# Kernel tuning notes

Measured on AMD Instinct MI355X. Metric: run time of the kernel, lower is better.

Reference implementation:

```python
import jax, jax.numpy as jnp
import numpy as np

B, T, C = 16, 64, 512


def setup_inputs() -> dict:
    key = jax.random.key(0)
    ks = jax.random.split(key, 12)
    s = 1.0 / np.sqrt(C)
    st = 1.0 / np.sqrt(2.0)
    return {
        "x": jax.random.normal(ks[0], (B, T, C), dtype=jnp.float32),
        "ts": jax.random.uniform(ks[1], (B, T), dtype=jnp.float32),
        "attn_mask": jnp.ones((B, T), dtype=jnp.float32),
        # project: Linear(C, C)
        "W_proj": jax.random.uniform(ks[2], (C, C), jnp.float32, -s, s),
        "b_proj": jax.random.uniform(ks[3], (C,), jnp.float32, -s, s),
        # embed_xs: Linear(C, C)
        "W_x": jax.random.uniform(ks[4], (C, C), jnp.float32, -s, s),
        "b_x": jax.random.uniform(ks[5], (C,), jnp.float32, -s, s),
        # embed_ts: Linear(2, C)
        "W_t": jax.random.uniform(ks[6], (2, C), jnp.float32, -st, st),
        "b_t": jax.random.uniform(ks[7], (C,), jnp.float32, -st, st),
        # get_importances Linear(C, C)
        "W_imp": jax.random.uniform(ks[8], (C, C), jnp.float32, -s, s),
        "b_imp": jax.random.uniform(ks[9], (C,), jnp.float32, -s, s),
    }


def reference(x, ts, attn_mask, W_proj, b_proj, W_x, b_x, W_t, b_t, W_imp, b_imp):
    # x: [B,T,C], ts: [B,T], attn_mask: [B,T]
    values = (x @ W_proj + b_proj)[:, None, :, :]          # [B,1,T,C]
    rel = ts[:, :, None] - ts[:, None, :]                  # [B,T,T]
    rel2 = jnp.log1p(jnp.maximum(jnp.stack([rel, -rel], axis=-1), 0.0))  # [B,T,T,2]
    h = rel2 @ W_t + b_t                                   # [B,T,T,C] (include_t)
    h = h + (x @ W_x + b_x)[:, None, :, :]                 # include_x, broadcast over dim 1
    importances = jax.nn.sigmoid(jax.nn.relu(h) @ W_imp + b_imp)  # [B,T,T,C]
    importances = importances * attn_mask[:, None, :, None]
    interactions = jax.nn.logsumexp(values * importances, axis=2)  # [B,T,C]
    return (x + interactions, importances.mean(axis=3))
```

## Files before the change

kernel.cpp:

```cpp
#include <hip/hip_runtime.h>
#include <hip/hip_bf16.h>

#define Bn 16
#define Tn 64
#define Cn 512
#define LDA 520

#define LOG2E 1.4426950408889634f
#define LN2   0.6931471805599453f

typedef short s8v __attribute__((ext_vector_type(8)));
typedef float f4v __attribute__((ext_vector_type(4)));

__device__ __forceinline__ unsigned short f2bf(float f){
  union { float f; unsigned int u; } c; c.f = f;
  return (unsigned short)((c.u + 0x7FFFu + ((c.u >> 16) & 1u)) >> 16);
}
__device__ __forceinline__ unsigned int pk2bf(float a, float b){
  __hip_bfloat162 t = __float22bfloat162_rn(make_float2(a, b));
  union { __hip_bfloat162 h; unsigned int u; } c; c.h = t; return c.u;
}
__device__ __forceinline__ float bits2f(unsigned int u){
  union { unsigned int u; float f; } c; c.u = u; return c.f;
}

__global__ void swz(const float* __restrict__ Wp, const float* __restrict__ Wx,
                    const float* __restrict__ Wi, const float* __restrict__ ts,
                    unsigned short* __restrict__ dstall, float* __restrict__ R){
  if(blockIdx.x < 384){
    int gid = blockIdx.x * 256 + threadIdx.x;
    int mat = gid >> 15;
    int rem = gid & 32767;
    int lane = rem & 63;
    int st   = rem >> 6;
    int t    = st & 31;
    int s    = st >> 5;
    int n  = t * 16 + (lane & 15);
    int k0 = s * 32 + ((lane >> 4) << 3);
    const float* W = (mat == 0) ? Wp : ((mat == 1) ? Wx : Wi);
    unsigned int p[4];
#pragma unroll
    for(int q = 0; q < 4; ++q)
      p[q] = pk2bf(W[(k0 + 2*q) * Cn + n], W[(k0 + 2*q + 1) * Cn + n]);
    uint4 o; o.x = p[0]; o.y = p[1]; o.z = p[2]; o.w = p[3];
    *reinterpret_cast<uint4*>(dstall + (size_t)mat * 262144 + (size_t)rem * 8) = o;
  } else {
    int gid2 = (blockIdx.x - 384) * 256 + threadIdx.x;
    float r[8];
#pragma unroll
    for(int q = 0; q < 4; ++q){
      int p = gid2 * 4 + q;
      int b = p >> 12, i = (p >> 6) & 63, j = p & 63;
      float d = ts[b * Tn + i] - ts[b * Tn + j];
      r[2*q]   = __logf(1.f + fmaxf(d, 0.f));
      r[2*q+1] = __logf(1.f + fmaxf(-d, 0.f));
    }
    float4* Rf4 = reinterpret_cast<float4*>(R);
    Rf4[gid2 * 2    ] = make_float4(r[0], r[1], r[2], r[3]);
    Rf4[gid2 * 2 + 1] = make_float4(r[4], r[5], r[6], r[7]);
  }
}

__global__ __launch_bounds__(256, 4)
void prep(const float* __restrict__ x, const float* __restrict__ bp,
          const float* __restrict__ bx, const float* __restrict__ bt,
          const unsigned short* __restrict__ WswP,
          const unsigned short* __restrict__ WswX,
          float* __restrict__ xe, unsigned short* __restrict__ vfrag){
  __shared__ unsigned short lA[Tn * LDA];
  const int b = blockIdx.x >> 2, mat = (blockIdx.x >> 1) & 1, half = blockIdx.x & 1;
  const int tid = threadIdx.x;
  const int c0 = (tid & 127) * 4, jb = tid >> 7;
#pragma unroll
  for(int it = 0; it < 32; ++it){
    int j = jb + it * 2;
    f4v xv = *reinterpret_cast<const f4v*>(x + ((b * Tn + j) * Cn + c0));
    uint2 uu; uu.x = pk2bf(xv[0], xv[1]); uu.y = pk2bf(xv[2], xv[3]);
    *reinterpret_cast<uint2*>(&lA[j * LDA + c0]) = uu;
  }
  __syncthreads();
  const unsigned short* Wsw = mat ? WswX : WswP;
  const int lane = tid & 63, w2 = tid >> 6, quad = lane >> 4, ln = lane & 15;
  const int wg = half * 4 + w2;
  f4v acc[4][4];
#pragma unroll
  for(int mt = 0; mt < 4; ++mt)
#pragma unroll
    for(int nt = 0; nt < 4; ++nt){
      acc[mt][nt][0] = 0.f; acc[mt][nt][1] = 0.f; acc[mt][nt][2] = 0.f; acc[mt][nt][3] = 0.f;
    }
#pragma unroll 1
  for(int s = 0; s < 16; ++s){
    s8v af[4], bfv[4];
#pragma unroll
    for(int mt = 0; mt < 4; ++mt)
      af[mt] = *reinterpret_cast<const s8v*>(&lA[(mt * 16 + ln) * LDA + s * 32 + quad * 8]);
#pragma unroll
    for(int nt = 0; nt < 4; ++nt)
      bfv[nt] = *reinterpret_cast<const s8v*>(Wsw + (((s * 32) + (wg * 4 + nt)) * 64 + lane) * 8);
#pragma unroll
    for(int mt = 0; mt < 4; ++mt)
#pragma unroll
      for(int nt = 0; nt < 4; ++nt)
        acc[mt][nt] = __builtin_amdgcn_mfma_f32_16x16x32_bf16(af[mt], bfv[nt], acc[mt][nt], 0, 0, 0);
  }
  if(mat == 0){
#pragma unroll
    for(int eb = 0; eb < 8; ++eb){
      int mt = eb >> 1, ntb = (eb & 1) * 2;
      unsigned int wds[4];
#pragma unroll
      for(int h = 0; h < 2; ++h){
        int nt = ntb + h;
        float bb = bp[wg * 64 + nt * 16 + ln];
        float v0 = (acc[mt][nt][0] + bb) * LOG2E;
        float v1 = (acc[mt][nt][1] + bb) * LOG2E;
        float v2 = (acc[mt][nt][2] + bb) * LOG2E;
        float v3 = (acc[mt][nt][3] + bb) * LOG2E;
        wds[h*2]   = pk2bf(v0, v1);
        wds[h*2+1] = pk2bf(v2, v3);
      }
      uint4 o; o.x = wds[0]; o.y = wds[1]; o.z = wds[2]; o.w = wds[3];
      *reinterpret_cast<uint4*>(vfrag + ((size_t)((b * 8 + wg) * 8 + eb) * 64 + lane) * 8) = o;
    }
  } else {
#pragma unroll
    for(int nt = 0; nt < 4; ++nt){
      int c = wg * 64 + nt * 16 + ln;
      float bb = bx[c] + bt[c];
#pragma unroll
      for(int mt = 0; mt < 4; ++mt)
#pragma unroll
        for(int r = 0; r < 4; ++r){
          int j = mt * 16 + quad * 4 + r;
          xe[(b * Tn + j) * Cn + c] = acc[mt][nt][r] + bb;
        }
    }
  }
}

__global__ __launch_bounds__(512, 4)
void fused(const float* __restrict__ x, const float* __restrict__ am,
           const float* __restrict__ Wt, const float* __restrict__ bimp,
           const unsigned short* __restrict__ Wsw, const float* __restrict__ R,
           const float* __restrict__ xe, const unsigned short* __restrict__ vfrag,
           float* __restrict__ out0, float* __restrict__ out1){
  __shared__ unsigned short lA[Tn * LDA];
  __shared__ float msk[Tn], rr0[Tn], rr1[Tn], rsum[Tn];
  const int b = blockIdx.x >> 6, i = blockIdx.x & 63;
  const int tid = threadIdx.x;
  if(tid < Tn){
    msk[tid] = am[b * Tn + tid];
    rsum[tid] = 0.f;
    float2 rv = reinterpret_cast<const float2*>(R)[(b * Tn + i) * Tn + tid];
    rr0[tid] = rv.x; rr1[tid] = rv.y;
  }
  __syncthreads();
  const int c0 = (tid & 127) * 4, jb = tid >> 7;
  f4v wt0 = *reinterpret_cast<const f4v*>(Wt + c0);
  f4v wt1 = *reinterpret_cast<const f4v*>(Wt + Cn + c0);
#pragma unroll
  for(int it = 0; it < 16; ++it){
    int j = jb + it * 4;
    float r0 = rr0[j], r1 = rr1[j];
    f4v xv = *reinterpret_cast<const f4v*>(xe + ((b * Tn + j) * Cn + c0));
    float h0 = fmaxf(fmaf(r1, wt1[0], fmaf(r0, wt0[0], xv[0])), 0.f);
    float h1 = fmaxf(fmaf(r1, wt1[1], fmaf(r0, wt0[1], xv[1])), 0.f);
    float h2 = fmaxf(fmaf(r1, wt1[2], fmaf(r0, wt0[2], xv[2])), 0.f);
    float h3 = fmaxf(fmaf(r1, wt1[3], fmaf(r0, wt0[3], xv[3])), 0.f);
    uint2 uu; uu.x = pk2bf(h0, h1); uu.y = pk2bf(h2, h3);
    *reinterpret_cast<uint2*>(&lA[j * LDA + c0]) = uu;
  }
  __syncthreads();

  const int lane = tid & 63, w = tid >> 6, quad = lane >> 4, ln = lane & 15;
  f4v acc[4][4];
#pragma unroll
  for(int mt = 0; mt < 4; ++mt)
#pragma unroll
    for(int nt = 0; nt < 4; ++nt){
      acc[mt][nt][0] = 0.f; acc[mt][nt][1] = 0.f; acc[mt][nt][2] = 0.f; acc[mt][nt][3] = 0.f;
    }
#pragma unroll 1
  for(int s = 0; s < 16; ++s){
    s8v af[4], bfv[4];
#pragma unroll
    for(int mt = 0; mt < 4; ++mt)
      af[mt] = *reinterpret_cast<const s8v*>(&lA[(mt * 16 + ln) * LDA + s * 32 + quad * 8]);
#pragma unroll
    for(int nt = 0; nt < 4; ++nt)
      bfv[nt] = *reinterpret_cast<const s8v*>(Wsw + (((s * 32) + (w * 4 + nt)) * 64 + lane) * 8);
#pragma unroll
    for(int mt = 0; mt < 4; ++mt)
#pragma unroll
      for(int nt = 0; nt < 4; ++nt)
        acc[mt][nt] = __builtin_amdgcn_mfma_f32_16x16x32_bf16(af[mt], bfv[nt], acc[mt][nt], 0, 0, 0);
  }

  uint4 vv[8];
#pragma unroll
  for(int eb = 0; eb < 8; ++eb)
    vv[eb] = *reinterpret_cast<const uint4*>(vfrag + ((size_t)((b * 8 + w) * 8 + eb) * 64 + lane) * 8);

  float bb[4];
#pragma unroll
  for(int nt = 0; nt < 4; ++nt) bb[nt] = bimp[w * 64 + nt * 16 + ln];
#pragma unroll
  for(int mt = 0; mt < 4; ++mt)
#pragma unroll
    for(int r = 0; r < 4; ++r){
      float mk = msk[mt * 16 + quad * 4 + r];
      float p = 0.f;
#pragma unroll
      for(int nt = 0; nt < 4; ++nt){
        float z = acc[mt][nt][r] + bb[nt];
        float im = mk * __builtin_amdgcn_rcpf(1.f + __builtin_amdgcn_exp2f(z * -LOG2E));
        acc[mt][nt][r] = im;
        p += im;
      }
      p += __shfl_xor(p, 1, 64);
      p += __shfl_xor(p, 2, 64);
      p += __shfl_xor(p, 4, 64);
      p += __shfl_xor(p, 8, 64);
      if(ln == 0) atomicAdd(&rsum[mt * 16 + quad * 4 + r], p);
    }
  __syncthreads();
  if(tid < Tn) out1[(b * Tn + i) * Tn + tid] = rsum[tid] * (1.f / 512.f);

  const unsigned int* vw = reinterpret_cast<const unsigned int*>(vv);
#pragma unroll
  for(int nt = 0; nt < 4; ++nt){
    float se = 0.f;
#pragma unroll
    for(int mt = 0; mt < 4; ++mt)
#pragma unroll
      for(int r = 0; r < 4; ++r){
        int e = mt * 16 + nt * 4 + r;
        unsigned int d = vw[e >> 1];
        float vl = bits2f((e & 1) ? (d & 0xffff0000u) : (d << 16));
        se += __builtin_amdgcn_exp2f(vl * acc[mt][nt][r]);
      }
    se += __shfl_xor(se, 16, 64);
    se += __shfl_xor(se, 32, 64);
    if(quad == 0){
      int idx = (b * Tn + i) * Cn + (w * 64 + nt * 16 + ln);
      out0[idx] = x[idx] + __builtin_amdgcn_logf(se) * LN2;
    }
  }
}

extern "C" void kernel_launch(void* const* d_in, const int* in_sizes, int n_in,
                              void* d_out, int out_size, void* d_ws, size_t ws_size,
                              hipStream_t stream){
  const float* x    = (const float*)d_in[0];
  const float* ts   = (const float*)d_in[1];
  const float* am   = (const float*)d_in[2];
  const float* Wp   = (const float*)d_in[3];
  const float* bp   = (const float*)d_in[4];
  const float* Wx   = (const float*)d_in[5];
  const float* bx   = (const float*)d_in[6];
  const float* Wt   = (const float*)d_in[7];
  const float* bt   = (const float*)d_in[8];
  const float* Wi   = (const float*)d_in[9];
  const float* bimp = (const float*)d_in[10];
  float* out0 = (float*)d_out;
  float* out1 = out0 + Bn * Tn * Cn;

  char* ws = (char*)d_ws;
  unsigned short* Wsw   = (unsigned short*)ws;
  float*          xe    = (float*)(ws + 3 * 524288);
  unsigned short* vfrag = (unsigned short*)(ws + 3*524288 + 2097152);
  float*          R     = (float*)(ws + 3*524288 + 2097152 + 1048576);

  swz<<<448, 256, 0, stream>>>(Wp, Wx, Wi, ts, Wsw, R);
  prep<<<64, 256, 0, stream>>>(x, bp, bx, bt, Wsw, Wsw + 262144, xe, vfrag);
  fused<<<1024, 512, 0, stream>>>(x, am, Wt, bimp, Wsw + 2 * 262144, R,
                                  xe, vfrag, out0, out1);
}
```

Measured before the change: 135.1 us.

## Switch importance GEMM to FP8 MFMA with scaling and software-pipelined loads

The main fused kernel's C×C importance GEMM now uses fp8 inputs (relu activations and W_imp quantized with scale factors) and the fp8 MFMA instruction, with the scales undone in the sigmoid input. The prep kernel is re-split across 4x more blocks with one N-tile per wave, and both GEMM loops now prefetch the next K-step's A and B fragments. This halves operand bytes and doubles MFMA throughput for the dominant GEMM, at the cost of reduced precision in the importances and outputs.

```diff
diff --git a/kernel.cpp b/kernel.cpp
--- a/kernel.cpp
+++ b/kernel.cpp
@@ -4,18 +4,19 @@
 #define Bn 16
 #define Tn 64
 #define Cn 512
-#define LDA 520
+#define LDA  520
+#define LDA8 528
 
 #define LOG2E 1.4426950408889634f
 #define LN2   0.6931471805599453f
+#define ASC 16.0f
+#define WSC 256.0f
+#define ZSC (1.0f/4096.0f)
 
 typedef short s8v __attribute__((ext_vector_type(8)));
 typedef float f4v __attribute__((ext_vector_type(4)));
-
-__device__ __forceinline__ unsigned short f2bf(float f){
-  union { float f; unsigned int u; } c; c.f = f;
-  return (unsigned short)((c.u + 0x7FFFu + ((c.u >> 16) & 1u)) >> 16);
-}
+typedef unsigned long ul2 __attribute__((ext_vector_type(2)));
+
 __device__ __forceinline__ unsigned int pk2bf(float a, float b){
   __hip_bfloat162 t = __float22bfloat162_rn(make_float2(a, b));
   union { __hip_bfloat162 h; unsigned int u; } c; c.h = t; return c.u;
@@ -26,26 +27,38 @@
 
 __global__ void swz(const float* __restrict__ Wp, const float* __restrict__ Wx,
                     const float* __restrict__ Wi, const float* __restrict__ ts,
-                    unsigned short* __restrict__ dstall, float* __restrict__ R){
-  if(blockIdx.x < 384){
-    int gid = blockIdx.x * 256 + threadIdx.x;
-    int mat = gid >> 15;
-    int rem = gid & 32767;
-    int lane = rem & 63;
-    int st   = rem >> 6;
-    int t    = st & 31;
-    int s    = st >> 5;
+                    unsigned short* __restrict__ WswB, unsigned char* __restrict__ Wsw8,
+                    float* __restrict__ R){
+  int blk = blockIdx.x;
+  if(blk < 256){
+    int gid = blk * 256 + threadIdx.x;
+    int mat = gid >> 15, rem = gid & 32767;
+    int lane = rem & 63, st = rem >> 6, t = st & 31, s = st >> 5;
     int n  = t * 16 + (lane & 15);
     int k0 = s * 32 + ((lane >> 4) << 3);
-    const float* W = (mat == 0) ? Wp : ((mat == 1) ? Wx : Wi);
+    const float* W = mat ? Wx : Wp;
     unsigned int p[4];
 #pragma unroll
     for(int q = 0; q < 4; ++q)
       p[q] = pk2bf(W[(k0 + 2*q) * Cn + n], W[(k0 + 2*q + 1) * Cn + n]);
     uint4 o; o.x = p[0]; o.y = p[1]; o.z = p[2]; o.w = p[3];
-    *reinterpret_cast<uint4*>(dstall + (size_t)mat * 262144 + (size_t)rem * 8) = o;
+    *reinterpret_cast<uint4*>(WswB + (size_t)mat * 262144 + (size_t)rem * 8) = o;
+  } else if(blk < 384){
+    int rem = (blk - 256) * 256 + threadIdx.x;
+    int nt = rem & 3, lane = (rem >> 2) & 63, w8 = (rem >> 8) & 7, s = rem >> 11;
+    int n  = (w8 * 4 + nt) * 16 + (lane & 15);
+    int k0 = s * 32 + ((lane >> 4) << 3);
+    float v[8];
+#pragma unroll
+    for(int j = 0; j < 8; ++j) v[j] = Wi[(k0 + j) * Cn + n] * WSC;
+    int d0 = __builtin_amdgcn_cvt_pk_fp8_f32(v[0], v[1], 0, false);
+    d0     = __builtin_amdgcn_cvt_pk_fp8_f32(v[2], v[3], d0, true);
+    int d1 = __builtin_amdgcn_cvt_pk_fp8_f32(v[4], v[5], 0, false);
+    d1     = __builtin_amdgcn_cvt_pk_fp8_f32(v[6], v[7], d1, true);
+    uint2 o; o.x = (unsigned int)d0; o.y = (unsigned int)d1;
+    *reinterpret_cast<uint2*>(Wsw8 + (size_t)((s * 8 + w8) * 64 + lane) * 32 + nt * 8) = o;
   } else {
-    int gid2 = (blockIdx.x - 384) * 256 + threadIdx.x;
+    int gid2 = (blk - 384) * 256 + threadIdx.x;
     float r[8];
 #pragma unroll
     for(int q = 0; q < 4; ++q){
@@ -61,15 +74,21 @@
   }
 }
 
-__global__ __launch_bounds__(256, 4)
+__global__ __launch_bounds__(256)
 void prep(const float* __restrict__ x, const float* __restrict__ bp,
           const float* __restrict__ bx, const float* __restrict__ bt,
-          const unsigned short* __restrict__ WswP,
-          const unsigned short* __restrict__ WswX,
+          const unsigned short* __restrict__ WswB,
           float* __restrict__ xe, unsigned short* __restrict__ vfrag){
   __shared__ unsigned short lA[Tn * LDA];
-  const int b = blockIdx.x >> 2, mat = (blockIdx.x >> 1) & 1, half = blockIdx.x & 1;
+  const int blk = blockIdx.x;
+  const int b = blk >> 4, mat = (blk >> 3) & 1, oct = blk & 7;
   const int tid = threadIdx.x;
+  const int lane = tid & 63, w2 = tid >> 6, quad = lane >> 4, ln = lane & 15;
+  const int t = oct * 4 + w2;
+
+  const s8v* Bp = reinterpret_cast<const s8v*>(WswB + (size_t)mat * 262144) + (t * 64 + lane);
+  s8v bcur = Bp[0];
+
   const int c0 = (tid & 127) * 4, jb = tid >> 7;
 #pragma unroll
   for(int it = 0; it < 32; ++it){
@@ -79,73 +98,63 @@
     *reinterpret_cast<uint2*>(&lA[j * LDA + c0]) = uu;
   }
   __syncthreads();
-  const unsigned short* Wsw = mat ? WswX : WswP;
-  const int lane = tid & 63, w2 = tid >> 6, quad = lane >> 4, ln = lane & 15;
-  const int wg = half * 4 + w2;
-  f4v acc[4][4];
+
+  s8v a[4], an[4];
 #pragma unroll
   for(int mt = 0; mt < 4; ++mt)
-#pragma unroll
-    for(int nt = 0; nt < 4; ++nt){
-      acc[mt][nt][0] = 0.f; acc[mt][nt][1] = 0.f; acc[mt][nt][2] = 0.f; acc[mt][nt][3] = 0.f;
-    }
-#pragma unroll 1
+    a[mt] = *reinterpret_cast<const s8v*>(&lA[(mt * 16 + ln) * LDA + quad * 8]);
+  f4v acc[4];
+#pragma unroll
+  for(int mt = 0; mt < 4; ++mt){ acc[mt][0]=0.f; acc[mt][1]=0.f; acc[mt][2]=0.f; acc[mt][3]=0.f; }
+
+#pragma unroll 2
   for(int s = 0; s < 16; ++s){
-    s8v af[4], bfv[4];
-#pragma unroll
-    for(int mt = 0; mt < 4; ++mt)
-      af[mt] = *reinterpret_cast<const s8v*>(&lA[(mt * 16 + ln) * LDA + s * 32 + quad * 8]);
-#pragma unroll
-    for(int nt = 0; nt < 4; ++nt)
-      bfv[nt] = *reinterpret_cast<const s8v*>(Wsw + (((s * 32) + (wg * 4 + nt)) * 64 + lane) * 8);
-#pragma unroll
-    for(int mt = 0; mt < 4; ++mt)
-#pragma unroll
-      for(int nt = 0; nt < 4; ++nt)
-        acc[mt][nt] = __builtin_amdgcn_mfma_f32_16x16x32_bf16(af[mt], bfv[nt], acc[mt][nt], 0, 0, 0);
-  }
+    int sn = (s + 1) & 15;
+    s8v bn = Bp[sn * 2048];
+#pragma unroll
+    for(int mt = 0; mt < 4; ++mt)
+      an[mt] = *reinterpret_cast<const s8v*>(&lA[(mt * 16 + ln) * LDA + sn * 32 + quad * 8]);
+#pragma unroll
+    for(int mt = 0; mt < 4; ++mt)
+      acc[mt] = __builtin_amdgcn_mfma_f32_16x16x32_bf16(a[mt], bcur, acc[mt], 0, 0, 0);
+#pragma unroll
+    for(int mt = 0; mt < 4; ++mt) a[mt] = an[mt];
+    bcur = bn;
+  }
+
+  const int c = t * 16 + ln;
   if(mat == 0){
-#pragma unroll
-    for(int eb = 0; eb < 8; ++eb){
-      int mt = eb >> 1, ntb = (eb & 1) * 2;
-      unsigned int wds[4];
-#pragma unroll
-      for(int h = 0; h < 2; ++h){
-        int nt = ntb + h;
-        float bb = bp[wg * 64 + nt * 16 + ln];
-        float v0 = (acc[mt][nt][0] + bb) * LOG2E;
-        float v1 = (acc[mt][nt][1] + bb) * LOG2E;
-        float v2 = (acc[mt][nt][2] + bb) * LOG2E;
-        float v3 = (acc[mt][nt][3] + bb) * LOG2E;
-        wds[h*2]   = pk2bf(v0, v1);
-        wds[h*2+1] = pk2bf(v2, v3);
+    float bb = bp[c];
+    const int eb_h = w2 & 1;
+#pragma unroll
+    for(int mt = 0; mt < 4; ++mt){
+      float v0 = (acc[mt][0] + bb) * LOG2E;
+      float v1 = (acc[mt][1] + bb) * LOG2E;
+      float v2 = (acc[mt][2] + bb) * LOG2E;
+      float v3 = (acc[mt][3] + bb) * LOG2E;
+      uint2 o; o.x = pk2bf(v0, v1); o.y = pk2bf(v2, v3);
+      int eb = mt * 2 + (w2 >> 1);
+      *reinterpret_cast<uint2*>(vfrag + ((size_t)((b * 8 + oct) * 8 + eb) * 64 + lane) * 8 + eb_h * 4) = o;
+    }
+  } else {
+    float bb = bx[c] + bt[c];
+#pragma unroll
+    for(int mt = 0; mt < 4; ++mt)
+#pragma unroll
+      for(int r = 0; r < 4; ++r){
+        int j = mt * 16 + quad * 4 + r;
+        xe[(b * Tn + j) * Cn + c] = (acc[mt][r] + bb) * ASC;
       }
-      uint4 o; o.x = wds[0]; o.y = wds[1]; o.z = wds[2]; o.w = wds[3];
-      *reinterpret_cast<uint4*>(vfrag + ((size_t)((b * 8 + wg) * 8 + eb) * 64 + lane) * 8) = o;
-    }
-  } else {
-#pragma unroll
-    for(int nt = 0; nt < 4; ++nt){
-      int c = wg * 64 + nt * 16 + ln;
-      float bb = bx[c] + bt[c];
-#pragma unroll
-      for(int mt = 0; mt < 4; ++mt)
-#pragma unroll
-        for(int r = 0; r < 4; ++r){
-          int j = mt * 16 + quad * 4 + r;
-          xe[(b * Tn + j) * Cn + c] = acc[mt][nt][r] + bb;
-        }
-    }
   }
 }
 
 __global__ __launch_bounds__(512, 4)
 void fused(const float* __restrict__ x, const float* __restrict__ am,
            const float* __restrict__ Wt, const float* __restrict__ bimp,
-           const unsigned short* __restrict__ Wsw, const float* __restrict__ R,
+           const unsigned char* __restrict__ Wsw8, const float* __restrict__ R,
            const float* __restrict__ xe, const unsigned short* __restrict__ vfrag,
            float* __restrict__ out0, float* __restrict__ out1){
-  __shared__ unsigned short lA[Tn * LDA];
+  __shared__ unsigned char lA8[Tn * LDA8];
   __shared__ float msk[Tn], rr0[Tn], rr1[Tn], rsum[Tn];
   const int b = blockIdx.x >> 6, i = blockIdx.x & 63;
   const int tid = threadIdx.x;
@@ -156,9 +165,17 @@
     rr0[tid] = rv.x; rr1[tid] = rv.y;
   }
   __syncthreads();
+
+  const int lane = tid & 63, w = tid >> 6, quad = lane >> 4, ln = lane & 15;
+  const ul2* Bv = reinterpret_cast<const ul2*>(Wsw8);
+  const int off = (w * 64 + lane) * 2;
+  ul2 b01 = Bv[off], b23 = Bv[off + 1];
+
   const int c0 = (tid & 127) * 4, jb = tid >> 7;
   f4v wt0 = *reinterpret_cast<const f4v*>(Wt + c0);
   f4v wt1 = *reinterpret_cast<const f4v*>(Wt + Cn + c0);
+  wt0[0]*=ASC; wt0[1]*=ASC; wt0[2]*=ASC; wt0[3]*=ASC;
+  wt1[0]*=ASC; wt1[1]*=ASC; wt1[2]*=ASC; wt1[3]*=ASC;
 #pragma unroll
   for(int it = 0; it < 16; ++it){
     int j = jb + it * 4;
@@ -168,33 +185,43 @@
     float h1 = fmaxf(fmaf(r1, wt1[1], fmaf(r0, wt0[1], xv[1])), 0.f);
     float h2 = fmaxf(fmaf(r1, wt1[2], fmaf(r0, wt0[2], xv[2])), 0.f);
     float h3 = fmaxf(fmaf(r1, wt1[3], fmaf(r0, wt0[3], xv[3])), 0.f);
-    uint2 uu; uu.x = pk2bf(h0, h1); uu.y = pk2bf(h2, h3);
-    *reinterpret_cast<uint2*>(&lA[j * LDA + c0]) = uu;
+    int d = __builtin_amdgcn_cvt_pk_fp8_f32(h0, h1, 0, false);
+    d     = __builtin_amdgcn_cvt_pk_fp8_f32(h2, h3, d, true);
+    *reinterpret_cast<int*>(lA8 + j * LDA8 + c0) = d;
   }
   __syncthreads();
 
-  const int lane = tid & 63, w = tid >> 6, quad = lane >> 4, ln = lane & 15;
+  unsigned long a[4], an[4];
+#pragma unroll
+  for(int mt = 0; mt < 4; ++mt)
+    a[mt] = *reinterpret_cast<const unsigned long*>(lA8 + (mt * 16 + ln) * LDA8 + quad * 8);
   f4v acc[4][4];
 #pragma unroll
   for(int mt = 0; mt < 4; ++mt)
 #pragma unroll
     for(int nt = 0; nt < 4; ++nt){
-      acc[mt][nt][0] = 0.f; acc[mt][nt][1] = 0.f; acc[mt][nt][2] = 0.f; acc[mt][nt][3] = 0.f;
-    }
-#pragma unroll 1
+      acc[mt][nt][0]=0.f; acc[mt][nt][1]=0.f; acc[mt][nt][2]=0.f; acc[mt][nt][3]=0.f;
+    }
+
+#pragma unroll 2
   for(int s = 0; s < 16; ++s){
-    s8v af[4], bfv[4];
-#pragma unroll
-    for(int mt = 0; mt < 4; ++mt)
-      af[mt] = *reinterpret_cast<const s8v*>(&lA[(mt * 16 + ln) * LDA + s * 32 + quad * 8]);
-#pragma unroll
-    for(int nt = 0; nt < 4; ++nt)
-      bfv[nt] = *reinterpret_cast<const s8v*>(Wsw + (((s * 32) + (w * 4 + nt)) * 64 + lane) * 8);
-#pragma unroll
-    for(int mt = 0; mt < 4; ++mt)
-#pragma unroll
-      for(int nt = 0; nt < 4; ++nt)
-        acc[mt][nt] = __builtin_amdgcn_mfma_f32_16x16x32_bf16(af[mt], bfv[nt], acc[mt][nt], 0, 0, 0);
+    int sn = (s + 1) & 15;
+    ul2 nb01 = Bv[sn * 1024 + off];
+    ul2 nb23 = Bv[sn * 1024 + off + 1];
+#pragma unroll
+    for(int mt = 0; mt < 4; ++mt)
+      an[mt] = *reinterpret_cast<const unsigned long*>(lA8 + (mt * 16 + ln) * LDA8 + sn * 32 + quad * 8);
+    long bf0 = (long)b01.x, bf1 = (long)b01.y, bf2 = (long)b23.x, bf3 = (long)b23.y;
+#pragma unroll
+    for(int mt = 0; mt < 4; ++mt){
+      acc[mt][0] = __builtin_amdgcn_mfma_f32_16x16x32_fp8_fp8((long)a[mt], bf0, acc[mt][0], 0, 0, 0);
+      acc[mt][1] = __builtin_amdgcn_mfma_f32_16x16x32_fp8_fp8((long)a[mt], bf1, acc[mt][1], 0, 0, 0);
+      acc[mt][2] = __builtin_amdgcn_mfma_f32_16x16x32_fp8_fp8((long)a[mt], bf2, acc[mt][2], 0, 0, 0);
+      acc[mt][3] = __builtin_amdgcn_mfma_f32_16x16x32_fp8_fp8((long)a[mt], bf3, acc[mt][3], 0, 0, 0);
+    }
+#pragma unroll
+    for(int mt = 0; mt < 4; ++mt) a[mt] = an[mt];
+    b01 = nb01; b23 = nb23;
   }
 
   uint4 vv[8];
@@ -213,7 +240,7 @@
       float p = 0.f;
 #pragma unroll
       for(int nt = 0; nt < 4; ++nt){
-        float z = acc[mt][nt][r] + bb[nt];
+        float z = fmaf(acc[mt][nt][r], ZSC, bb[nt]);
         float im = mk * __builtin_amdgcn_rcpf(1.f + __builtin_amdgcn_exp2f(z * -LOG2E));
         acc[mt][nt][r] = im;
         p += im;
@@ -267,13 +294,13 @@
   float* out1 = out0 + Bn * Tn * Cn;
 
   char* ws = (char*)d_ws;
-  unsigned short* Wsw   = (unsigned short*)ws;
-  float*          xe    = (float*)(ws + 3 * 524288);
-  unsigned short* vfrag = (unsigned short*)(ws + 3*524288 + 2097152);
-  float*          R     = (float*)(ws + 3*524288 + 2097152 + 1048576);
-
-  swz<<<448, 256, 0, stream>>>(Wp, Wx, Wi, ts, Wsw, R);
-  prep<<<64, 256, 0, stream>>>(x, bp, bx, bt, Wsw, Wsw + 262144, xe, vfrag);
-  fused<<<1024, 512, 0, stream>>>(x, am, Wt, bimp, Wsw + 2 * 262144, R,
-                                  xe, vfrag, out0, out1);
-}
+  unsigned short* WswB  = (unsigned short*)ws;
+  unsigned char*  Wsw8  = (unsigned char*)(ws + 1048576);
+  float*          xe    = (float*)(ws + 1310720);
+  unsigned short* vfrag = (unsigned short*)(ws + 3407872);
+  float*          R     = (float*)(ws + 4456448);
+
+  swz<<<448, 256, 0, stream>>>(Wp, Wx, Wi, ts, WswB, Wsw8, R);
+  prep<<<256, 256, 0, stream>>>(x, bp, bx, bt, WswB, xe, vfrag);
+  fused<<<1024, 512, 0, stream>>>(x, am, Wt, bimp, Wsw8, R, xe, vfrag, out0, out1);
+}
```

Result: faster. 126.3 us (-6.5%).
